# Performance work log

Measured on AMD Instinct MI355X. Metric: run time of the kernel, lower is better.

## Reference

```python
import jax, jax.numpy as jnp
import numpy as np

B, N, D_IN = 2, 2048, 2048
D_OUT, H, KV = 2048, 32, 8
G = H // KV          # group_size = 4
DH = D_OUT // H      # head dim = 64


def setup_inputs() -> dict:
    key = jax.random.key(0)
    k0, k1, k2, k3, k4, k5 = jax.random.split(key, 6)
    s_in = 1.0 / np.sqrt(D_IN)
    s_out = 1.0 / np.sqrt(D_OUT)
    return {
        "x": jax.random.normal(k0, (B, N, D_IN), dtype=jnp.float32),
        "Wq": jax.random.normal(k1, (D_IN, H * DH), dtype=jnp.float32) * s_in,
        "Wk": jax.random.normal(k2, (D_IN, KV * DH), dtype=jnp.float32) * s_in,
        "Wv": jax.random.normal(k3, (D_IN, KV * DH), dtype=jnp.float32) * s_in,
        "Wo": jax.random.normal(k4, (D_OUT, D_IN), dtype=jnp.float32) * s_out,
        "bo": jax.random.normal(k5, (D_IN,), dtype=jnp.float32) * 0.01,
    }


def gqa_forward(x, Wq, Wk, Wv, Wo, bo):
    b, n, _ = x.shape
    scale = 1.0 / jnp.sqrt(jnp.asarray(DH, x.dtype))
    # projections
    q = (x @ Wq).reshape(b, n, KV, G, DH)   # queries grouped by shared kv head
    k = (x @ Wk).reshape(b, n, KV, DH)
    v = (x @ Wv).reshape(b, n, KV, DH)
    # scores: (B, KV, G, N, N) — equivalent to repeat_interleave of K over groups
    scores = jnp.einsum('bnkgd,bmkd->bkgnm', q, k) * scale
    causal = jnp.triu(jnp.ones((n, n), dtype=bool), k=1)
    scores = jnp.where(causal, -jnp.inf, scores)
    attn = jax.nn.softmax(scores, axis=-1)
    # dropout p=0.0 -> identity
    ctx = jnp.einsum('bkgnm,bmkd->bnkgd', attn, v).reshape(b, n, D_OUT)
    return ctx @ Wo + bo


def reference(x, Wq, Wk, Wv, Wo, bo):
    return gqa_forward(x, Wq, Wk, Wv, Wo, bo)
```

## Files before the change

kernel.cpp:

```cpp
#include <hip/hip_runtime.h>
#include <hip/hip_bf16.h>
#include <cstdint>


#define B_    2
#define N_    2048
#define DIN_  2048
#define H_    32
#define KV_   8
#define DH_   64
#define M_    4096
#define NQKV_ 3072

typedef float f32x4 __attribute__((ext_vector_type(4)));
typedef __bf16 bf16x8 __attribute__((ext_vector_type(8)));
typedef unsigned short u16x8 __attribute__((ext_vector_type(8)));

__device__ __forceinline__ unsigned short f32_to_bf16_bits(float f) {
  unsigned int u = __float_as_uint(f);
  u = (u + 0x7FFFu + ((u >> 16) & 1u)) >> 16;
  return (unsigned short)u;
}

__device__ __forceinline__ void gload_lds16(const void* g, void* l) {
  __builtin_amdgcn_global_load_lds(
      (__attribute__((address_space(1))) void*)(g),
      (__attribute__((address_space(3))) void*)(l), 16, 0, 0);
}

__global__ __launch_bounds__(256) void prep(
    const float* __restrict__ x, const float* __restrict__ Wq,
    const float* __restrict__ Wk, const float* __restrict__ Wv,
    const float* __restrict__ Wo,
    unsigned short* __restrict__ Xb, unsigned short* __restrict__ Wqkv,
    unsigned short* __restrict__ Wot, float qscale) {
  const int task = blockIdx.y, tid = threadIdx.x;
  if (task == 0) {
    size_t i0 = ((size_t)blockIdx.x * 256 + tid) * 2;
#pragma unroll
    for (int t = 0; t < 2; ++t) {
      float4 v = ((const float4*)x)[i0 + t];
      ushort4 o;
      o.x = f32_to_bf16_bits(v.x);
      o.y = f32_to_bf16_bits(v.y);
      o.z = f32_to_bf16_bits(v.z);
      o.w = f32_to_bf16_bits(v.w);
      ((ushort4*)Xb)[i0 + t] = o;
    }
    return;
  }
  const float* src;
  unsigned short* dst;
  int NC, off;
  float scale = 1.0f;
  switch (task) {
    case 1: src = Wq; dst = Wqkv; NC = 2048; off = 0;    scale = qscale; break;
    case 2: src = Wk; dst = Wqkv; NC = 512;  off = 2048; break;
    case 3: src = Wv; dst = Wqkv; NC = 512;  off = 2560; break;
    default: src = Wo; dst = Wot; NC = 2048; off = 0;    break;
  }
  const int nx = NC >> 5;
  const int bx = blockIdx.x;
  if (bx >= nx * 64) return;
  const int n0 = (bx % nx) * 32, k0 = (bx / nx) * 32;
  __shared__ float tile[32][33];
  const int tx = tid & 31, ty = tid >> 5;
#pragma unroll
  for (int i = 0; i < 32; i += 8)
    tile[ty + i][tx] = src[(size_t)(k0 + ty + i) * NC + n0 + tx];
  __syncthreads();
#pragma unroll
  for (int i = 0; i < 32; i += 8)
    dst[(size_t)(off + n0 + ty + i) * 2048 + k0 + tx] =
        f32_to_bf16_bits(tile[tx][ty + i] * scale);
}

__global__ __launch_bounds__(256) void transpose_v(
    const unsigned short* __restrict__ QKV, unsigned short* __restrict__ Vtg) {
  __shared__ unsigned short t[64][72];
  int nt = blockIdx.x, bkv = blockIdx.y;
  int b = bkv >> 3, kv = bkv & 7;
  int tid = threadIdx.x;
  int row = tid >> 2, c = (tid & 3) * 16;
  const unsigned short* src =
      QKV + (size_t)(b * N_ + nt * 64 + row) * NQKV_ + 2560 + kv * 64;
  *(u16x8*)&t[row][c]     = *(const u16x8*)(src + c);
  *(u16x8*)&t[row][c + 8] = *(const u16x8*)(src + c + 8);
  __syncthreads();
  int d = tid >> 2;
  unsigned short* dst = Vtg + ((size_t)bkv * 64 + d) * N_ + nt * 64 + c;
  u16x8 o0, o1;
#pragma unroll
  for (int i = 0; i < 8; ++i) { o0[i] = t[c + i][d]; o1[i] = t[c + 8 + i][d]; }
  *(u16x8*)dst = o0;
  *(u16x8*)(dst + 8) = o1;
}

template <bool OUT_BF16, bool BIAS>
__global__ __launch_bounds__(256, 3) void gemm_bt(
    const unsigned short* __restrict__ A,
    const unsigned short* __restrict__ Bt,
    void* __restrict__ Cv,
    const float* __restrict__ bias,
    int Nn, int K) {
  __shared__ unsigned short As[128 * 32];
  __shared__ unsigned short Bs[128 * 32];

  const int tid = threadIdx.x;
  const int lane = tid & 63;
  const int wave = tid >> 6;
  const int wm = wave >> 1, wn = wave & 1;
  const int l16 = lane & 15, quad = lane >> 4;
  const int m0 = blockIdx.y * 128, n0 = blockIdx.x * 128;

  f32x4 acc[4][4] = {};

  const int srow = tid >> 2;
  const int kc = tid & 3;

  for (int kk = 0; kk < K; kk += 32) {
#pragma unroll
    for (int c = 0; c < 2; ++c) {
      int r = c * 64 + srow;
      int ofs = r * 32 + kc * 8;
      gload_lds16(A + (size_t)(m0 + r) * K + kk + kc * 8, (char*)As + ofs * 2);
      gload_lds16(Bt + (size_t)(n0 + r) * K + kk + kc * 8, (char*)Bs + ofs * 2);
    }
    __syncthreads();
    bf16x8 af[4], bfr[4];
#pragma unroll
    for (int mi = 0; mi < 4; ++mi)
      af[mi] = *(const bf16x8*)&As[(wm * 64 + mi * 16 + l16) * 32 + quad * 8];
#pragma unroll
    for (int ni = 0; ni < 4; ++ni)
      bfr[ni] = *(const bf16x8*)&Bs[(wn * 64 + ni * 16 + l16) * 32 + quad * 8];
#pragma unroll
    for (int mi = 0; mi < 4; ++mi)
#pragma unroll
      for (int ni = 0; ni < 4; ++ni)
        acc[mi][ni] = __builtin_amdgcn_mfma_f32_16x16x32_bf16(
            af[mi], bfr[ni], acc[mi][ni], 0, 0, 0);
    __syncthreads();
  }

  unsigned short* Cb = (unsigned short*)Cv;
  float* Cf = (float*)Cv;
#pragma unroll
  for (int mi = 0; mi < 4; ++mi) {
    int rrow = m0 + wm * 64 + mi * 16 + quad * 4;
#pragma unroll
    for (int ni = 0; ni < 4; ++ni) {
      int col = n0 + wn * 64 + ni * 16 + l16;
      float bv = BIAS ? bias[col] : 0.0f;
#pragma unroll
      for (int r = 0; r < 4; ++r) {
        float v = acc[mi][ni][r] + bv;
        if (OUT_BF16)
          Cb[(size_t)(rrow + r) * Nn + col] = f32_to_bf16_bits(v);
        else
          Cf[(size_t)(rrow + r) * Nn + col] = v;
      }
    }
  }
}

__global__ __launch_bounds__(256, 1) void attn_fwd(
    const unsigned short* __restrict__ QKV,
    const unsigned short* __restrict__ Vtg,
    unsigned short* __restrict__ Ctx) {
  __shared__ unsigned short Ks[2][64 * 64];
  __shared__ unsigned short Vs[2][64 * 64];
  __shared__ unsigned short Ps[4][4][16 * 64];

  const int p = blockIdx.x;
  const int kv = blockIdx.y, b = blockIdx.z;
  const int tid = threadIdx.x, lane = tid & 63, wave = tid >> 6;
  const int l16 = lane & 15, quad = lane >> 4;
  const int h = kv * 4 + wave;
  const size_t baserow = (size_t)b * N_;
  const unsigned short* Kg = QKV + 2048 + kv * 64;
  const unsigned short* Vg = Vtg + (size_t)(b * KV_ + kv) * 64 * N_;
  const int sw = l16 & 7;

  auto stageKV = [&](int j, int buf) {
#pragma unroll
    for (int it = 0; it < 2; ++it) {
      int c = tid + it * 256;
      int row = c >> 3, off = ((c & 7) ^ (row & 7)) * 8;
      gload_lds16(Kg + (baserow + j * 64 + row) * NQKV_ + off,
                  (char*)Ks[buf] + c * 16);
      gload_lds16(Vg + (size_t)row * N_ + j * 64 + off,
                  (char*)Vs[buf] + c * 16);
    }
  };

#pragma unroll 1
  for (int phase = 0; phase < 2; ++phase) {
    const int qtile = phase ? p : 31 - p;
    const int q0 = qtile * 64;

    bf16x8 qa[4][2];
#pragma unroll
    for (int s = 0; s < 4; ++s)
#pragma unroll
      for (int ks = 0; ks < 2; ++ks)
        qa[s][ks] = *(const bf16x8*)(QKV +
            (baserow + q0 + s * 16 + l16) * NQKV_ + h * 64 + ks * 32 + quad * 8);

    f32x4 oacc[4][4] = {};
    float lp[4][4] = {};

    __syncthreads();
    stageKV(0, 0);

    for (int j = 0; j <= qtile; ++j) {
      __syncthreads();
      const int buf = j & 1;
      if (j < qtile) stageKV(j + 1, buf ^ 1);

      bf16x8 kb[2][4];
#pragma unroll
      for (int ks = 0; ks < 2; ++ks)
#pragma unroll
        for (int ni = 0; ni < 4; ++ni)
          kb[ks][ni] = *(const bf16x8*)&Ks[buf][(ni * 16 + l16) * 64 +
                                               ((ks * 4 + quad) ^ sw) * 8];

#pragma unroll
      for (int s = 0; s < 4; ++s) {
        f32x4 sc[4] = {};
#pragma unroll
        for (int ks = 0; ks < 2; ++ks)
#pragma unroll
          for (int ni = 0; ni < 4; ++ni)
            sc[ni] = __builtin_amdgcn_mfma_f32_16x16x32_bf16(
                qa[s][ks], kb[ks][ni], sc[ni], 0, 0, 0);
        if (j == qtile) {
          const int qrow = q0 + s * 16 + quad * 4;
#pragma unroll
          for (int ni = 0; ni < 4; ++ni) {
            int kcol = q0 + ni * 16 + l16;
#pragma unroll
            for (int r = 0; r < 4; ++r)
              if (kcol > qrow + r) sc[ni][r] = -1e30f;
          }
        }
        unsigned short* Pw = &Ps[wave][s][0];
#pragma unroll
        for (int ni = 0; ni < 4; ++ni) {
          const int cl = ni * 2 + (l16 >> 3);
#pragma unroll
          for (int r = 0; r < 4; ++r) {
            float pe = __builtin_amdgcn_exp2f(sc[ni][r]);
            lp[s][r] += pe;
            int row = quad * 4 + r;
            Pw[row * 64 + ((cl ^ (row & 7)) * 8) + (l16 & 7)] =
                (unsigned short)(__float_as_uint(pe) >> 16);
          }
        }
      }

      bf16x8 vb[2][4];
#pragma unroll
      for (int ks = 0; ks < 2; ++ks)
#pragma unroll
        for (int di = 0; di < 4; ++di)
          vb[ks][di] = *(const bf16x8*)&Vs[buf][(di * 16 + l16) * 64 +
                                               ((ks * 4 + quad) ^ sw) * 8];
#pragma unroll
      for (int s = 0; s < 4; ++s) {
        bf16x8 pa[2];
#pragma unroll
        for (int ks = 0; ks < 2; ++ks)
          pa[ks] = *(const bf16x8*)&Ps[wave][s][l16 * 64 + ((ks * 4 + quad) ^ sw) * 8];
#pragma unroll
        for (int ks = 0; ks < 2; ++ks)
#pragma unroll
          for (int di = 0; di < 4; ++di)
            oacc[s][di] = __builtin_amdgcn_mfma_f32_16x16x32_bf16(
                pa[ks], vb[ks][di], oacc[s][di], 0, 0, 0);
      }
    }

#pragma unroll
    for (int s = 0; s < 4; ++s) {
      float inv[4];
#pragma unroll
      for (int r = 0; r < 4; ++r) {
        float v = lp[s][r];
#pragma unroll
        for (int off = 1; off < 16; off <<= 1) v += __shfl_xor(v, off);
        inv[r] = 1.0f / v;
      }
#pragma unroll
      for (int di = 0; di < 4; ++di)
#pragma unroll
        for (int r = 0; r < 4; ++r) {
          size_t row = baserow + q0 + s * 16 + quad * 4 + r;
          Ctx[row * 2048 + h * 64 + di * 16 + l16] =
              f32_to_bf16_bits(oacc[s][di][r] * inv[r]);
        }
    }
  }
}

extern "C" void kernel_launch(void* const* d_in, const int* in_sizes, int n_in,
                              void* d_out, int out_size, void* d_ws, size_t ws_size,
                              hipStream_t stream) {
  const float* x  = (const float*)d_in[0];
  const float* Wq = (const float*)d_in[1];
  const float* Wk = (const float*)d_in[2];
  const float* Wv = (const float*)d_in[3];
  const float* Wo = (const float*)d_in[4];
  const float* bo = (const float*)d_in[5];
  float* out = (float*)d_out;

  unsigned short* Xb   = (unsigned short*)d_ws;
  unsigned short* Wqkv = Xb + (size_t)M_ * DIN_;
  unsigned short* QKV  = Wqkv + (size_t)NQKV_ * DIN_;
  unsigned short* Wot  = QKV + (size_t)M_ * NQKV_;
  unsigned short* Ctx  = Xb;
  unsigned short* Vtg  = Wqkv;

  const float kQScale = 0.125f * 1.44269504088896340736f;

  prep<<<dim3(4096, 5), 256, 0, stream>>>(x, Wq, Wk, Wv, Wo, Xb, Wqkv, Wot, kQScale);

  gemm_bt<true, false><<<dim3(NQKV_ / 128, M_ / 128), 256, 0, stream>>>(
      Xb, Wqkv, QKV, nullptr, NQKV_, DIN_);

  transpose_v<<<dim3(N_ / 64, B_ * KV_), 256, 0, stream>>>(QKV, Vtg);

  attn_fwd<<<dim3(16, 8, 2), 256, 0, stream>>>(QKV, Vtg, Ctx);

  gemm_bt<false, true><<<dim3(DIN_ / 128, M_ / 128), 256, 0, stream>>>(
      Ctx, Wot, out, bo, DIN_, 2048);
}
```

Measured before the change: 307.3 us.

## Halve attention query tile, double grid, and load K/V directly into registers

The attention kernel now gives each block 32-row query tiles instead of 64, launches twice as many blocks, and allows two blocks per CU. K and V tiles are read from global memory straight into registers, with K double-buffered in registers, instead of being staged through LDS with barriers. The aim is more parallelism and occupancy, and no block-level synchronization in the inner loop. The cost is that each of the four waves now issues its own global K/V loads instead of sharing one LDS copy, which adds memory traffic, and masking now works on 32-row halves within 64-key tiles.

```diff
diff --git a/kernel.cpp b/kernel.cpp
--- a/kernel.cpp
+++ b/kernel.cpp
@@ -164,13 +164,11 @@
   }
 }
 
-__global__ __launch_bounds__(256, 1) void attn_fwd(
+__global__ __launch_bounds__(256, 2) void attn_fwd(
     const unsigned short* __restrict__ QKV,
     const unsigned short* __restrict__ Vtg,
     unsigned short* __restrict__ Ctx) {
-  __shared__ unsigned short Ks[2][64 * 64];
-  __shared__ unsigned short Vs[2][64 * 64];
-  __shared__ unsigned short Ps[4][4][16 * 64];
+  __shared__ unsigned short Ps[4][2][16 * 64];
 
   const int p = blockIdx.x;
   const int kv = blockIdx.y, b = blockIdx.z;
@@ -178,68 +176,68 @@
   const int l16 = lane & 15, quad = lane >> 4;
   const int h = kv * 4 + wave;
   const size_t baserow = (size_t)b * N_;
-  const unsigned short* Kg = QKV + 2048 + kv * 64;
-  const unsigned short* Vg = Vtg + (size_t)(b * KV_ + kv) * 64 * N_;
+  const unsigned short* Kbase = QKV + baserow * NQKV_ + 2048 + kv * 64;
+  const unsigned short* Vbase = Vtg + (size_t)(b * KV_ + kv) * 64 * N_;
+  const unsigned short* Qbase = QKV + baserow * NQKV_ + h * 64;
   const int sw = l16 & 7;
 
-  auto stageKV = [&](int j, int buf) {
-#pragma unroll
-    for (int it = 0; it < 2; ++it) {
-      int c = tid + it * 256;
-      int row = c >> 3, off = ((c & 7) ^ (row & 7)) * 8;
-      gload_lds16(Kg + (baserow + j * 64 + row) * NQKV_ + off,
-                  (char*)Ks[buf] + c * 16);
-      gload_lds16(Vg + (size_t)row * N_ + j * 64 + off,
-                  (char*)Vs[buf] + c * 16);
-    }
+  auto loadK = [&](int j, bf16x8 (&kb)[2][4]) {
+#pragma unroll
+    for (int ks = 0; ks < 2; ++ks)
+#pragma unroll
+      for (int i = 0; i < 4; ++i)
+        kb[ks][i] = *(const bf16x8*)(Kbase +
+            (size_t)(j * 64 + i * 16 + l16) * NQKV_ + ks * 32 + quad * 8);
+  };
+  auto loadV = [&](int j, bf16x8 (&vb)[2][4]) {
+#pragma unroll
+    for (int ks = 0; ks < 2; ++ks)
+#pragma unroll
+      for (int i = 0; i < 4; ++i)
+        vb[ks][i] = *(const bf16x8*)(Vbase +
+            (size_t)(i * 16 + l16) * N_ + j * 64 + ks * 32 + quad * 8);
   };
 
 #pragma unroll 1
   for (int phase = 0; phase < 2; ++phase) {
-    const int qtile = phase ? p : 31 - p;
-    const int q0 = qtile * 64;
-
-    bf16x8 qa[4][2];
-#pragma unroll
-    for (int s = 0; s < 4; ++s)
+    const int ih = phase ? p : 63 - p;
+    const int q0 = ih * 32;
+    const int nt = (ih >> 1) + 1;
+
+    bf16x8 qa[2][2];
+#pragma unroll
+    for (int s = 0; s < 2; ++s)
 #pragma unroll
       for (int ks = 0; ks < 2; ++ks)
-        qa[s][ks] = *(const bf16x8*)(QKV +
-            (baserow + q0 + s * 16 + l16) * NQKV_ + h * 64 + ks * 32 + quad * 8);
-
-    f32x4 oacc[4][4] = {};
-    float lp[4][4] = {};
-
-    __syncthreads();
-    stageKV(0, 0);
-
-    for (int j = 0; j <= qtile; ++j) {
-      __syncthreads();
-      const int buf = j & 1;
-      if (j < qtile) stageKV(j + 1, buf ^ 1);
-
-      bf16x8 kb[2][4];
-#pragma unroll
-      for (int ks = 0; ks < 2; ++ks)
-#pragma unroll
-        for (int ni = 0; ni < 4; ++ni)
-          kb[ks][ni] = *(const bf16x8*)&Ks[buf][(ni * 16 + l16) * 64 +
-                                               ((ks * 4 + quad) ^ sw) * 8];
-
-#pragma unroll
-      for (int s = 0; s < 4; ++s) {
+        qa[s][ks] = *(const bf16x8*)(Qbase +
+            (size_t)(q0 + s * 16 + l16) * NQKV_ + ks * 32 + quad * 8);
+
+    f32x4 oacc[2][4] = {};
+    float lp[2][4] = {};
+
+    bf16x8 kb[2][2][4], vb[2][4];
+    loadK(0, kb[0]);
+
+#pragma unroll 2
+    for (int j = 0; j < nt; ++j) {
+      const int cur = j & 1;
+      if (j + 1 < nt) loadK(j + 1, kb[cur ^ 1]);
+      loadV(j, vb);
+
+#pragma unroll
+      for (int s = 0; s < 2; ++s) {
         f32x4 sc[4] = {};
 #pragma unroll
         for (int ks = 0; ks < 2; ++ks)
 #pragma unroll
           for (int ni = 0; ni < 4; ++ni)
             sc[ni] = __builtin_amdgcn_mfma_f32_16x16x32_bf16(
-                qa[s][ks], kb[ks][ni], sc[ni], 0, 0, 0);
-        if (j == qtile) {
+                qa[s][ks], kb[cur][ks][ni], sc[ni], 0, 0, 0);
+        if (j == nt - 1) {
           const int qrow = q0 + s * 16 + quad * 4;
 #pragma unroll
           for (int ni = 0; ni < 4; ++ni) {
-            int kcol = q0 + ni * 16 + l16;
+            int kcol = j * 64 + ni * 16 + l16;
 #pragma unroll
             for (int r = 0; r < 4; ++r)
               if (kcol > qrow + r) sc[ni][r] = -1e30f;
@@ -259,16 +257,8 @@
           }
         }
       }
-
-      bf16x8 vb[2][4];
-#pragma unroll
-      for (int ks = 0; ks < 2; ++ks)
-#pragma unroll
-        for (int di = 0; di < 4; ++di)
-          vb[ks][di] = *(const bf16x8*)&Vs[buf][(di * 16 + l16) * 64 +
-                                               ((ks * 4 + quad) ^ sw) * 8];
-#pragma unroll
-      for (int s = 0; s < 4; ++s) {
+#pragma unroll
+      for (int s = 0; s < 2; ++s) {
         bf16x8 pa[2];
 #pragma unroll
         for (int ks = 0; ks < 2; ++ks)
@@ -283,7 +273,7 @@
     }
 
 #pragma unroll
-    for (int s = 0; s < 4; ++s) {
+    for (int s = 0; s < 2; ++s) {
       float inv[4];
 #pragma unroll
       for (int r = 0; r < 4; ++r) {
@@ -331,7 +321,7 @@
 
   transpose_v<<<dim3(N_ / 64, B_ * KV_), 256, 0, stream>>>(QKV, Vtg);
 
-  attn_fwd<<<dim3(16, 8, 2), 256, 0, stream>>>(QKV, Vtg, Ctx);
+  attn_fwd<<<dim3(32, 8, 2), 256, 0, stream>>>(QKV, Vtg, Ctx);
 
   gemm_bt<false, true><<<dim3(DIN_ / 128, M_ / 128), 256, 0, stream>>>(
       Ctx, Wot, out, bo, DIN_, 2048);
```

After: 502.8 us. +63.6%, slower.
